# Performance work log

Measured on AMD Instinct MI355X. Metric: run time of the kernel, lower is better.

## Reference

```python
import jax, jax.numpy as jnp
import numpy as np

STEPS = 3


def setup_inputs() -> dict:
    key = jax.random.key(0)
    ks = jax.random.split(key, 6)
    N, H, B = 1000000, 128, 16384
    x = jax.random.normal(ks[0], (N, H), dtype=jnp.float32)
    batch_vec = jnp.sort(jax.random.randint(ks[1], (N,), 0, B)).astype(jnp.int64)
    scale_ih = 1.0 / np.sqrt(2 * H)
    scale_hh = 1.0 / np.sqrt(H)
    W_ih = jax.random.normal(ks[2], (4 * H, 2 * H), dtype=jnp.float32) * scale_ih
    W_hh = jax.random.normal(ks[3], (4 * H, H), dtype=jnp.float32) * scale_hh
    b_ih = jnp.zeros((4 * H,), dtype=jnp.float32)
    b_hh = jnp.zeros((4 * H,), dtype=jnp.float32)
    return {"x": x, "batch_vec": batch_vec, "W_ih": W_ih, "W_hh": W_hh,
            "b_ih": b_ih, "b_hh": b_hh, "num_graphs": B}


def _set2set(x, batch_vec, W_ih, W_hh, b_ih, b_hh, B):
    N, H = x.shape
    q_star = jnp.zeros((B, 2 * H), x.dtype)
    h = jnp.zeros((B, H), x.dtype)
    c = jnp.zeros((B, H), x.dtype)
    bias = b_ih + b_hh
    for _ in range(STEPS):
        # LSTMCell (torch gate order: i, f, g, o)
        gates = q_star @ W_ih.T + h @ W_hh.T + bias  # [B, 4H]
        i, f, g, o = jnp.split(gates, 4, axis=-1)
        c = jax.nn.sigmoid(f) * c + jax.nn.sigmoid(i) * jnp.tanh(g)
        h = jax.nn.sigmoid(o) * jnp.tanh(c)
        q = h  # [B, H]
        # attention logits per node
        e = jnp.sum(x * q[batch_vec], axis=-1)  # [N]
        emax = jax.ops.segment_max(e, batch_vec, num_segments=B)
        emax = jax.lax.stop_gradient(jnp.where(jnp.isfinite(emax), emax, 0.0))
        ex = jnp.exp(e - emax[batch_vec])
        denom = jax.ops.segment_sum(ex, batch_vec, num_segments=B)
        a = ex / denom[batch_vec]  # segment softmax, [N]
        r = jax.ops.segment_sum(a[:, None] * x, batch_vec, num_segments=B)  # [B, H]
        q_star = jnp.concatenate([q, r], axis=-1)  # [B, 2H]
    return q_star


def reference(x, batch_vec, W_ih, W_hh, b_ih, b_hh, num_graphs):
    return _set2set(x, batch_vec, W_ih, W_hh, b_ih, b_hh, int(num_graphs))
```

## Files before the change

### kernel.cpp

```cpp
#include <hip/hip_runtime.h>
#include <math.h>

#define HDIM 128
#define G4 512
#define TS 36

typedef float vf4 __attribute__((ext_vector_type(4)));
typedef unsigned short u16x8 __attribute__((ext_vector_type(8)));

__device__ __forceinline__ float sigm(float v) { return 1.0f / (1.0f + __expf(-v)); }
__device__ __forceinline__ float ftanh(float v) {
    return 1.0f - 2.0f / (__expf(2.0f * v) + 1.0f);
}
__device__ __forceinline__ float dot4(vf4 a, vf4 b) {
    return a.x * b.x + a.y * b.y + a.z * b.z + a.w * b.w;
}
__device__ __forceinline__ vf4 ldnt4(const float* p) {
    return __builtin_nontemporal_load((const vf4*)p);
}
__device__ __forceinline__ unsigned short f2bf(float f) {
    unsigned u = __float_as_uint(f);
    u += 0x7fff + ((u >> 16) & 1);
    return (unsigned short)(u >> 16);
}
__device__ __forceinline__ float bf2f(unsigned short h) {
    return __uint_as_float(((unsigned)h) << 16);
}

__global__ __launch_bounds__(256) void k_setup(const float* __restrict__ W_ih,
                                               const float* __restrict__ W_hh,
                                               const float* __restrict__ b_ih,
                                               const float* __restrict__ b_hh,
                                               const int* __restrict__ batch_vec, int N, int B,
                                               float* __restrict__ Wc, int* __restrict__ seg_start,
                                               float* __restrict__ gh0) {
    __shared__ float h0s[HDIM];
    int t = blockIdx.x * 256 + threadIdx.x;
    if (blockIdx.x < 2) {
        if (threadIdx.x < HDIM) {
            int hid = threadIdx.x;
            float bi = b_ih[hid] + b_hh[hid];
            float bg = b_ih[2 * HDIM + hid] + b_hh[2 * HDIM + hid];
            float bo = b_ih[3 * HDIM + hid] + b_hh[3 * HDIM + hid];
            float c0 = sigm(bi) * ftanh(bg);
            h0s[hid] = sigm(bo) * ftanh(c0);
        }
        __syncthreads();
        if (t < G4) {
            float s = 0.0f;
#pragma unroll
            for (int k = 0; k < HDIM; k += 4) {
                vf4 wi = *(const vf4*)(W_ih + (size_t)t * 256 + k);
                vf4 wh = *(const vf4*)(W_hh + (size_t)t * HDIM + k);
                s += (wi.x + wh.x) * h0s[k] + (wi.y + wh.y) * h0s[k + 1] +
                     (wi.z + wh.z) * h0s[k + 2] + (wi.w + wh.w) * h0s[k + 3];
            }
            gh0[t] = s;
        }
    }
    if (t < G4 * 2 * HDIM) {
        int g = t >> 8;
        int k = t & 255;
        float w = W_ih[g * 256 + k];
        if (k < HDIM) w += W_hh[g * HDIM + k];
        Wc[t] = w;
    }
    if (t <= B) {
        int lo = 0, hi = N;
        while (lo < hi) {
            int mid = (lo + hi) >> 1;
            if (batch_vec[mid] < t) lo = mid + 1; else hi = mid;
        }
        seg_start[t] = lo;
    }
}

#define UPD(m_, d_, ra_, rb_, p_, xa_, xb_)  \
    {                                        \
        float mn_ = fmaxf(m_, p_);           \
        float sc_ = __expf(m_ - mn_);        \
        float pe_ = __expf(p_ - mn_);        \
        d_ = d_ * sc_ + pe_;                 \
        ra_ = ra_ * sc_ + pe_ * xa_;         \
        rb_ = rb_ * sc_ + pe_ * xb_;         \
        m_ = mn_;                            \
    }

#define SHFL16(p_)                  \
    p_ += __shfl_xor(p_, 1, 64);    \
    p_ += __shfl_xor(p_, 2, 64);    \
    p_ += __shfl_xor(p_, 4, 64);    \
    p_ += __shfl_xor(p_, 8, 64);

struct AttState {
    float m0, d0, m1, d1;
    vf4 ra0, rb0, ra1, rb1;
};

__device__ __forceinline__ void init_state(AttState& st) {
    st.m0 = 0.f; st.d0 = 0.f; st.m1 = 0.f; st.d1 = 0.f;
    st.ra0 = vf4{0.f, 0.f, 0.f, 0.f}; st.rb0 = vf4{0.f, 0.f, 0.f, 0.f};
    st.ra1 = vf4{0.f, 0.f, 0.f, 0.f}; st.rb1 = vf4{0.f, 0.f, 0.f, 0.f};
}

__device__ __forceinline__ void compute4(const vf4 xa[4], const vf4 xb[4], int baserow, int e,
                                         vf4 qa, vf4 qb, AttState& st) {
    float p[4];
#pragma unroll
    for (int t = 0; t < 4; ++t) p[t] = dot4(xa[t], qa) + dot4(xb[t], qb);
    SHFL16(p[0]) SHFL16(p[1]) SHFL16(p[2]) SHFL16(p[3])
#pragma unroll
    for (int t = 0; t < 4; ++t)
        if (baserow + t >= e) p[t] = -1e30f;
    UPD(st.m0, st.d0, st.ra0, st.rb0, p[0], xa[0], xb[0])
    UPD(st.m1, st.d1, st.ra1, st.rb1, p[1], xa[1], xb[1])
    UPD(st.m0, st.d0, st.ra0, st.rb0, p[2], xa[2], xb[2])
    UPD(st.m1, st.d1, st.ra1, st.rb1, p[3], xa[3], xb[3])
}

__device__ __forceinline__ void finish_state(AttState& st, float* dst) {
    float M = fmaxf(st.m0, st.m1);
    float w0 = __expf(st.m0 - M), w1 = __expf(st.m1 - M);
    float d = st.d0 * w0 + st.d1 * w1;
    vf4 ra = st.ra0 * w0 + st.ra1 * w1;
    vf4 rb = st.rb0 * w0 + st.rb1 * w1;
    float inv = (d > 0.0f) ? 1.0f / d : 0.0f;
    *(vf4*)dst = ra * inv;
    *(vf4*)(dst + 4) = rb * inv;
}

__device__ __forceinline__ int seg_of_block(int bid, int nblk, int rev, int wave, int quarter) {
    int q8 = nblk >> 3, r8 = nblk & 7;
    int xcd = bid & 7, pos = bid >> 3;
    int nb = (xcd < r8 ? xcd * (q8 + 1) : r8 * (q8 + 1) + (xcd - r8) * q8) + pos;
    if (rev) nb = nblk - 1 - nb;
    return nb * 16 + wave * 4 + quarter;
}

__global__ __launch_bounds__(256) void k_attn_cvt(const float* __restrict__ x,
                                                  unsigned short* __restrict__ x16,
                                                  const float* __restrict__ b_ih,
                                                  const float* __restrict__ b_hh,
                                                  const int* __restrict__ seg_start,
                                                  float* __restrict__ r_out, int B) {
    int wave = threadIdx.x >> 6;
    int lane = threadIdx.x & 63;
    int l16 = lane & 15;
    int quarter = lane >> 4;
    int seg = seg_of_block(blockIdx.x, gridDim.x, 0, wave, quarter);
    int seg_c = min(seg, B - 1);
    int s = seg_start[seg_c], e = seg_start[seg_c + 1];
    if (seg >= B) { s = 0; e = 0; }

    vf4 qa, qb;
    {
        int c = l16 * 8;
        vf4 bi0 = *(const vf4*)(b_ih + c) + *(const vf4*)(b_hh + c);
        vf4 bi1 = *(const vf4*)(b_ih + c + 4) + *(const vf4*)(b_hh + c + 4);
        vf4 bg0 = *(const vf4*)(b_ih + 2 * HDIM + c) + *(const vf4*)(b_hh + 2 * HDIM + c);
        vf4 bg1 = *(const vf4*)(b_ih + 2 * HDIM + c + 4) + *(const vf4*)(b_hh + 2 * HDIM + c + 4);
        vf4 bo0 = *(const vf4*)(b_ih + 3 * HDIM + c) + *(const vf4*)(b_hh + 3 * HDIM + c);
        vf4 bo1 = *(const vf4*)(b_ih + 3 * HDIM + c + 4) + *(const vf4*)(b_hh + 3 * HDIM + c + 4);
#pragma unroll
        for (int j = 0; j < 4; ++j) {
            float c0 = sigm(bi0[j]) * ftanh(bg0[j]);
            qa[j] = sigm(bo0[j]) * ftanh(c0);
            float c1 = sigm(bi1[j]) * ftanh(bg1[j]);
            qb[j] = sigm(bo1[j]) * ftanh(c1);
        }
    }

    int iters = (e - s + 3) >> 2;
    iters = max(iters, __shfl_xor(iters, 16, 64));
    iters = max(iters, __shfl_xor(iters, 32, 64));
    iters = max(iters, 1);

    AttState st;
    init_state(st);

    vf4 ca[4], cb[4];
#pragma unroll
    for (int t = 0; t < 4; ++t) {
        int rl = max(min(s + t, e - 1), 0);
        const float* xr = x + (size_t)rl * HDIM + l16 * 8;
        ca[t] = ldnt4(xr);
        cb[t] = ldnt4(xr + 4);
    }
    int base = s;
#pragma unroll 1
    for (int j = 1; j < iters; ++j) {
        vf4 na[4], nb[4];
#pragma unroll
        for (int t = 0; t < 4; ++t) {
            int rl = max(min(s + 4 * j + t, e - 1), 0);
            const float* xr = x + (size_t)rl * HDIM + l16 * 8;
            na[t] = ldnt4(xr);
            nb[t] = ldnt4(xr + 4);
        }
#pragma unroll
        for (int t = 0; t < 4; ++t) {
            if (base + t < e) {
                u16x8 cv;
                cv[0] = f2bf(ca[t].x); cv[1] = f2bf(ca[t].y); cv[2] = f2bf(ca[t].z); cv[3] = f2bf(ca[t].w);
                cv[4] = f2bf(cb[t].x); cv[5] = f2bf(cb[t].y); cv[6] = f2bf(cb[t].z); cv[7] = f2bf(cb[t].w);
                *(u16x8*)(x16 + (size_t)(base + t) * HDIM + l16 * 8) = cv;
            }
        }
        compute4(ca, cb, base, e, qa, qb, st);
#pragma unroll
        for (int t = 0; t < 4; ++t) { ca[t] = na[t]; cb[t] = nb[t]; }
        base += 4;
    }
#pragma unroll
    for (int t = 0; t < 4; ++t) {
        if (base + t < e) {
            u16x8 cv;
            cv[0] = f2bf(ca[t].x); cv[1] = f2bf(ca[t].y); cv[2] = f2bf(ca[t].z); cv[3] = f2bf(ca[t].w);
            cv[4] = f2bf(cb[t].x); cv[5] = f2bf(cb[t].y); cv[6] = f2bf(cb[t].z); cv[7] = f2bf(cb[t].w);
            *(u16x8*)(x16 + (size_t)(base + t) * HDIM + l16 * 8) = cv;
        }
    }
    compute4(ca, cb, base, e, qa, qb, st);

    if (seg < B) finish_state(st, r_out + (size_t)seg * HDIM + l16 * 8);
}

__global__ __launch_bounds__(256) void k_attn_b16(const unsigned short* __restrict__ x16,
                                                  const float* __restrict__ q, int ldq,
                                                  const int* __restrict__ seg_start,
                                                  float* __restrict__ r_out, int ldr, int col_off,
                                                  int B, int rev) {
    int wave = threadIdx.x >> 6;
    int lane = threadIdx.x & 63;
    int l16 = lane & 15;
    int quarter = lane >> 4;
    int seg = seg_of_block(blockIdx.x, gridDim.x, rev, wave, quarter);
    int seg_c = min(seg, B - 1);
    int s = seg_start[seg_c], e = seg_start[seg_c + 1];
    if (seg >= B) { s = 0; e = 0; }

    const float* qrow = q + (size_t)seg_c * ldq + l16 * 8;
    vf4 qa = *(const vf4*)qrow;
    vf4 qb = *(const vf4*)(qrow + 4);

    int iters = (e - s + 3) >> 2;
    iters = max(iters, __shfl_xor(iters, 16, 64));
    iters = max(iters, __shfl_xor(iters, 32, 64));
    iters = max(iters, 1);

    AttState st;
    init_state(st);

    u16x8 cur[4];
#pragma unroll
    for (int t = 0; t < 4; ++t) {
        int rl = max(min(s + t, e - 1), 0);
        cur[t] = *(const u16x8*)(x16 + (size_t)rl * HDIM + l16 * 8);
    }
    int base = s;
#pragma unroll 1
    for (int j = 1; j < iters; ++j) {
        u16x8 nxt[4];
#pragma unroll
        for (int t = 0; t < 4; ++t) {
            int rl = max(min(s + 4 * j + t, e - 1), 0);
            nxt[t] = *(const u16x8*)(x16 + (size_t)rl * HDIM + l16 * 8);
        }
        vf4 xa[4], xb[4];
#pragma unroll
        for (int t = 0; t < 4; ++t) {
            xa[t] = vf4{bf2f(cur[t][0]), bf2f(cur[t][1]), bf2f(cur[t][2]), bf2f(cur[t][3])};
            xb[t] = vf4{bf2f(cur[t][4]), bf2f(cur[t][5]), bf2f(cur[t][6]), bf2f(cur[t][7])};
        }
        compute4(xa, xb, base, e, qa, qb, st);
#pragma unroll
        for (int t = 0; t < 4; ++t) cur[t] = nxt[t];
        base += 4;
    }
    {
        vf4 xa[4], xb[4];
#pragma unroll
        for (int t = 0; t < 4; ++t) {
            xa[t] = vf4{bf2f(cur[t][0]), bf2f(cur[t][1]), bf2f(cur[t][2]), bf2f(cur[t][3])};
            xb[t] = vf4{bf2f(cur[t][4]), bf2f(cur[t][5]), bf2f(cur[t][6]), bf2f(cur[t][7])};
        }
        compute4(xa, xb, base, e, qa, qb, st);
    }

    if (seg < B) finish_state(st, r_out + (size_t)seg * ldr + col_off + l16 * 8);
}

__global__ __launch_bounds__(256) void k_gemm_lstm1(const float* __restrict__ r_prev,
                                                    const float* __restrict__ Wc,
                                                    const float* __restrict__ gh0,
                                                    const float* __restrict__ b_ih,
                                                    const float* __restrict__ b_hh,
                                                    float* __restrict__ h_new,
                                                    float* __restrict__ c_new) {
    __shared__ float As[128 * TS];
    __shared__ float Ws[64 * TS];
    int ct = blockIdx.y;
    int rb = blockIdx.x * 128;
    int tid = threadIdx.x;
    int tx = tid & 15, ty = tid >> 4;
    float acc[8][4];
#pragma unroll
    for (int i = 0; i < 8; ++i)
#pragma unroll
        for (int j = 0; j < 4; ++j) acc[i][j] = 0.0f;

    for (int kc = 0; kc < 4; ++kc) {
        int kbase = kc * 32;
#pragma unroll
        for (int i = 0; i < 4; ++i) {
            int li = tid + i * 256;
            int row = li >> 3;
            int c4 = (li & 7) * 4;
            *(vf4*)&As[row * TS + c4] = *(const vf4*)(r_prev + (size_t)(rb + row) * HDIM + kbase + c4);
        }
#pragma unroll
        for (int i = 0; i < 2; ++i) {
            int li = tid + i * 256;
            int col = li >> 3;
            int c4 = (li & 7) * 4;
            int g = ct * 16 + (col & 15) + 128 * (col >> 4);
            *(vf4*)&Ws[col * TS + c4] = *(const vf4*)(Wc + (size_t)g * 256 + 128 + kbase + c4);
        }
        __syncthreads();
#pragma unroll
        for (int k = 0; k < 32; k += 4) {
            vf4 a[8], b[4];
#pragma unroll
            for (int i = 0; i < 8; ++i) a[i] = *(vf4*)&As[(ty + 16 * i) * TS + k];
#pragma unroll
            for (int j = 0; j < 4; ++j) b[j] = *(vf4*)&Ws[(tx + 16 * j) * TS + k];
#pragma unroll
            for (int i = 0; i < 8; ++i)
#pragma unroll
                for (int j = 0; j < 4; ++j) {
                    acc[i][j] += a[i].x * b[j].x + a[i].y * b[j].y +
                                 a[i].z * b[j].z + a[i].w * b[j].w;
                }
        }
        __syncthreads();
    }
    int hidx = ct * 16 + tx;
    float bi = b_ih[hidx] + b_hh[hidx] + gh0[hidx];
    float bf = b_ih[HDIM + hidx] + b_hh[HDIM + hidx] + gh0[HDIM + hidx];
    float bg = b_ih[2 * HDIM + hidx] + b_hh[2 * HDIM + hidx] + gh0[2 * HDIM + hidx];
    float bo = b_ih[3 * HDIM + hidx] + b_hh[3 * HDIM + hidx] + gh0[3 * HDIM + hidx];
    float bi0 = b_ih[hidx] + b_hh[hidx];
    float bg0 = b_ih[2 * HDIM + hidx] + b_hh[2 * HDIM + hidx];
    float c0 = sigm(bi0) * ftanh(bg0);
#pragma unroll
    for (int i = 0; i < 8; ++i) {
        int row = rb + ty + 16 * i;
        float gi = acc[i][0] + bi;
        float gf = acc[i][1] + bf;
        float gg = acc[i][2] + bg;
        float go = acc[i][3] + bo;
        float cn = sigm(gf) * c0 + sigm(gi) * ftanh(gg);
        float hn = sigm(go) * ftanh(cn);
        c_new[(size_t)row * HDIM + hidx] = cn;
        h_new[(size_t)row * HDIM + hidx] = hn;
    }
}

__global__ __launch_bounds__(256) void k_gemm_lstm(const float* __restrict__ h_prev,
                                                   const float* __restrict__ r_prev,
                                                   const float* __restrict__ c_prev,
                                                   const float* __restrict__ Wc,
                                                   const float* __restrict__ b_ih,
                                                   const float* __restrict__ b_hh,
                                                   float* __restrict__ h_mirror) {
    __shared__ float As[128 * TS];
    __shared__ float Ws[64 * TS];
    int ct = blockIdx.y;
    int rb = blockIdx.x * 128;
    int tid = threadIdx.x;
    int tx = tid & 15, ty = tid >> 4;
    float acc[8][4];
#pragma unroll
    for (int i = 0; i < 8; ++i)
#pragma unroll
        for (int j = 0; j < 4; ++j) acc[i][j] = 0.0f;

    for (int kc = 0; kc < 8; ++kc) {
        const float* src = (kc < 4) ? h_prev : r_prev;
        int kbase = (kc & 3) * 32;
#pragma unroll
        for (int i = 0; i < 4; ++i) {
            int li = tid + i * 256;
            int row = li >> 3;
            int c4 = (li & 7) * 4;
            *(vf4*)&As[row * TS + c4] = *(const vf4*)(src + (size_t)(rb + row) * HDIM + kbase + c4);
        }
#pragma unroll
        for (int i = 0; i < 2; ++i) {
            int li = tid + i * 256;
            int col = li >> 3;
            int c4 = (li & 7) * 4;
            int g = ct * 16 + (col & 15) + 128 * (col >> 4);
            *(vf4*)&Ws[col * TS + c4] = *(const vf4*)(Wc + (size_t)g * 256 + kc * 32 + c4);
        }
        __syncthreads();
#pragma unroll
        for (int k = 0; k < 32; k += 4) {
            vf4 a[8], b[4];
#pragma unroll
            for (int i = 0; i < 8; ++i) a[i] = *(vf4*)&As[(ty + 16 * i) * TS + k];
#pragma unroll
            for (int j = 0; j < 4; ++j) b[j] = *(vf4*)&Ws[(tx + 16 * j) * TS + k];
#pragma unroll
            for (int i = 0; i < 8; ++i)
#pragma unroll
                for (int j = 0; j < 4; ++j) {
                    acc[i][j] += a[i].x * b[j].x + a[i].y * b[j].y +
                                 a[i].z * b[j].z + a[i].w * b[j].w;
                }
        }
        __syncthreads();
    }
    int hidx = ct * 16 + tx;
    float bi = b_ih[hidx] + b_hh[hidx];
    float bf = b_ih[HDIM + hidx] + b_hh[HDIM + hidx];
    float bg = b_ih[2 * HDIM + hidx] + b_hh[2 * HDIM + hidx];
    float bo = b_ih[3 * HDIM + hidx] + b_hh[3 * HDIM + hidx];
#pragma unroll
    for (int i = 0; i < 8; ++i) {
        int row = rb + ty + 16 * i;
        float gi = acc[i][0] + bi;
        float gf = acc[i][1] + bf;
        float gg = acc[i][2] + bg;
        float go = acc[i][3] + bo;
        float cp = c_prev[(size_t)row * HDIM + hidx];
        float cn = sigm(gf) * cp + sigm(gi) * ftanh(gg);
        float hn = sigm(go) * ftanh(cn);
        h_mirror[(size_t)row * 2 * HDIM + hidx] = hn;
    }
}

extern "C" void kernel_launch(void* const* d_in, const int* in_sizes, int n_in,
                              void* d_out, int out_size, void* d_ws, size_t ws_size,
                              hipStream_t stream) {
    const float* x = (const float*)d_in[0];
    const int* batch_vec = (const int*)d_in[1];
    const float* W_ih = (const float*)d_in[2];
    const float* W_hh = (const float*)d_in[3];
    const float* b_ih = (const float*)d_in[4];
    const float* b_hh = (const float*)d_in[5];
    float* out = (float*)d_out;

    int N = in_sizes[1];
    int B = out_size / (2 * HDIM);

    char* ws = (char*)d_ws;
    float* Wc = (float*)ws;            ws += (size_t)G4 * 2 * HDIM * 4;
    float* gh0 = (float*)ws;           ws += (size_t)G4 * 4;
    float* h_b = (float*)ws;           ws += (size_t)B * HDIM * 4;
    float* cbuf = (float*)ws;          ws += (size_t)B * HDIM * 4;
    float* rbuf = (float*)ws;          ws += (size_t)B * HDIM * 4;
    int* seg = (int*)ws;               ws += (size_t)(B + 1) * 4;
    ws = (char*)(((size_t)ws + 255) & ~(size_t)255);
    unsigned short* x16 = (unsigned short*)ws;

    k_setup<<<512, 256, 0, stream>>>(W_ih, W_hh, b_ih, b_hh, batch_vec, N, B, Wc, seg, gh0);

    dim3 ggrid(B / 128, 8);
    int ablk = (B + 15) / 16;
    k_attn_cvt<<<ablk, 256, 0, stream>>>(x, x16, b_ih, b_hh, seg, rbuf, B);
    k_gemm_lstm1<<<ggrid, 256, 0, stream>>>(rbuf, Wc, gh0, b_ih, b_hh, h_b, cbuf);
    k_attn_b16<<<ablk, 256, 0, stream>>>(x16, h_b, HDIM, seg, rbuf, HDIM, 0, B, 1);
    k_gemm_lstm<<<ggrid, 256, 0, stream>>>(h_b, rbuf, cbuf, Wc, b_ih, b_hh, out);
    k_attn_b16<<<ablk, 256, 0, stream>>>(x16, out, 2 * HDIM, seg, out, 2 * HDIM, HDIM, B, 0);
}
```

Before: 456.4 us.

## Partition attention by fixed node slabs with atomic merging of straddling segments

Replaces the one-segment-per-16-lane-group attention kernels with kernels where each wave processes a fixed slab of 256 consecutive nodes and walks the segment boundaries inside it. Segments entirely inside a slab are written directly, and segments that cross slabs are merged with atomic adds into raw numerator and denominator buffers. Normalization moves into the following GEMM loads and a final small normalize kernel. This targets load imbalance from variable segment sizes and the padding waste in quarter-wave groups. In exchange it drops max-subtraction in the softmax, so exp can overflow on large logits, and it adds a memset, atomics and an extra kernel.

```diff
diff --git a/kernel.cpp b/kernel.cpp
--- a/kernel.cpp
+++ b/kernel.cpp
@@ -4,6 +4,8 @@
 #define HDIM 128
 #define G4 512
 #define TS 36
+#define SLAB 256
+#define WIN 16
 
 typedef float vf4 __attribute__((ext_vector_type(4)));
 typedef unsigned short u16x8 __attribute__((ext_vector_type(8)));
@@ -26,6 +28,12 @@
 __device__ __forceinline__ float bf2f(unsigned short h) {
     return __uint_as_float(((unsigned)h) << 16);
 }
+
+#define SHFL16(p_)                  \
+    p_ += __shfl_xor(p_, 1, 64);    \
+    p_ += __shfl_xor(p_, 2, 64);    \
+    p_ += __shfl_xor(p_, 4, 64);    \
+    p_ += __shfl_xor(p_, 8, 64);
 
 __global__ __launch_bounds__(256) void k_setup(const float* __restrict__ W_ih,
                                                const float* __restrict__ W_hh,
@@ -75,82 +83,59 @@
     }
 }
 
-#define UPD(m_, d_, ra_, rb_, p_, xa_, xb_)  \
-    {                                        \
-        float mn_ = fmaxf(m_, p_);           \
-        float sc_ = __expf(m_ - mn_);        \
-        float pe_ = __expf(p_ - mn_);        \
-        d_ = d_ * sc_ + pe_;                 \
-        ra_ = ra_ * sc_ + pe_ * xa_;         \
-        rb_ = rb_ * sc_ + pe_ * xb_;         \
-        m_ = mn_;                            \
-    }
-
-#define SHFL16(p_)                  \
-    p_ += __shfl_xor(p_, 1, 64);    \
-    p_ += __shfl_xor(p_, 2, 64);    \
-    p_ += __shfl_xor(p_, 4, 64);    \
-    p_ += __shfl_xor(p_, 8, 64);
-
-struct AttState {
-    float m0, d0, m1, d1;
-    vf4 ra0, rb0, ra1, rb1;
-};
-
-__device__ __forceinline__ void init_state(AttState& st) {
-    st.m0 = 0.f; st.d0 = 0.f; st.m1 = 0.f; st.d1 = 0.f;
-    st.ra0 = vf4{0.f, 0.f, 0.f, 0.f}; st.rb0 = vf4{0.f, 0.f, 0.f, 0.f};
-    st.ra1 = vf4{0.f, 0.f, 0.f, 0.f}; st.rb1 = vf4{0.f, 0.f, 0.f, 0.f};
-}
-
-__device__ __forceinline__ void compute4(const vf4 xa[4], const vf4 xb[4], int baserow, int e,
-                                         vf4 qa, vf4 qb, AttState& st) {
-    float p[4];
-#pragma unroll
-    for (int t = 0; t < 4; ++t) p[t] = dot4(xa[t], qa) + dot4(xb[t], qb);
-    SHFL16(p[0]) SHFL16(p[1]) SHFL16(p[2]) SHFL16(p[3])
-#pragma unroll
-    for (int t = 0; t < 4; ++t)
-        if (baserow + t >= e) p[t] = -1e30f;
-    UPD(st.m0, st.d0, st.ra0, st.rb0, p[0], xa[0], xb[0])
-    UPD(st.m1, st.d1, st.ra1, st.rb1, p[1], xa[1], xb[1])
-    UPD(st.m0, st.d0, st.ra0, st.rb0, p[2], xa[2], xb[2])
-    UPD(st.m1, st.d1, st.ra1, st.rb1, p[3], xa[3], xb[3])
-}
-
-__device__ __forceinline__ void finish_state(AttState& st, float* dst) {
-    float M = fmaxf(st.m0, st.m1);
-    float w0 = __expf(st.m0 - M), w1 = __expf(st.m1 - M);
-    float d = st.d0 * w0 + st.d1 * w1;
-    vf4 ra = st.ra0 * w0 + st.ra1 * w1;
-    vf4 rb = st.rb0 * w0 + st.rb1 * w1;
-    float inv = (d > 0.0f) ? 1.0f / d : 0.0f;
-    *(vf4*)dst = ra * inv;
-    *(vf4*)(dst + 4) = rb * inv;
-}
-
-__device__ __forceinline__ int seg_of_block(int bid, int nblk, int rev, int wave, int quarter) {
-    int q8 = nblk >> 3, r8 = nblk & 7;
-    int xcd = bid & 7, pos = bid >> 3;
-    int nb = (xcd < r8 ? xcd * (q8 + 1) : r8 * (q8 + 1) + (xcd - r8) * q8) + pos;
-    if (rev) nb = nblk - 1 - nb;
-    return nb * 16 + wave * 4 + quarter;
-}
-
-__global__ __launch_bounds__(256) void k_attn_cvt(const float* __restrict__ x,
-                                                  unsigned short* __restrict__ x16,
-                                                  const float* __restrict__ b_ih,
-                                                  const float* __restrict__ b_hh,
-                                                  const int* __restrict__ seg_start,
-                                                  float* __restrict__ r_out, int B) {
-    int wave = threadIdx.x >> 6;
-    int lane = threadIdx.x & 63;
-    int l16 = lane & 15;
-    int quarter = lane >> 4;
-    int seg = seg_of_block(blockIdx.x, gridDim.x, 0, wave, quarter);
-    int seg_c = min(seg, B - 1);
-    int s = seg_start[seg_c], e = seg_start[seg_c + 1];
-    if (seg >= B) { s = 0; e = 0; }
+__device__ __forceinline__ void flush_seg(int seg, int segLo, int segend, int r0, int r1,
+                                          float d, vf4 ra, vf4 rb,
+                                          float* __restrict__ r_raw, float* __restrict__ d_raw,
+                                          int l16, int quarter) {
+#pragma unroll
+    for (int off = 16; off <= 32; off <<= 1) {
+        d += __shfl_xor(d, off, 64);
+        ra.x += __shfl_xor(ra.x, off, 64);
+        ra.y += __shfl_xor(ra.y, off, 64);
+        ra.z += __shfl_xor(ra.z, off, 64);
+        ra.w += __shfl_xor(ra.w, off, 64);
+        rb.x += __shfl_xor(rb.x, off, 64);
+        rb.y += __shfl_xor(rb.y, off, 64);
+        rb.z += __shfl_xor(rb.z, off, 64);
+        rb.w += __shfl_xor(rb.w, off, 64);
+    }
+    if (quarter != 0) return;
+    float* rp = r_raw + (size_t)seg * HDIM + l16 * 8;
+    if (segLo >= r0 && segend <= r1) {
+        float inv = d > 0.f ? 1.f / d : 0.f;
+        *(vf4*)rp = ra * inv;
+        *(vf4*)(rp + 4) = rb * inv;
+        if (l16 == 0) d_raw[seg] = 1.0f;
+    } else {
+#pragma unroll
+        for (int j = 0; j < 4; ++j) {
+            atomicAdd(rp + j, ra[j]);
+            atomicAdd(rp + 4 + j, rb[j]);
+        }
+        if (l16 == 0) atomicAdd(d_raw + seg, d);
+    }
+}
+
+__global__ __launch_bounds__(256) void k_attn_lin32(const float* __restrict__ x,
+                                                    unsigned short* __restrict__ x16,
+                                                    const float* __restrict__ b_ih,
+                                                    const float* __restrict__ b_hh,
+                                                    const int* __restrict__ seg_start,
+                                                    float* __restrict__ r_raw,
+                                                    float* __restrict__ d_raw, int N, int B) {
+    int wave = threadIdx.x >> 6, lane = threadIdx.x & 63;
+    int l16 = lane & 15, quarter = lane >> 4;
+    int wid = blockIdx.x * 4 + wave;
+    int r0 = wid * SLAB;
+    if (r0 >= N) return;
+    int r1 = min(r0 + SLAB, N);
+
+    int lo = 0, hi = B - 1;
+    while (lo < hi) { int mid = (lo + hi + 1) >> 1; if (seg_start[mid] <= r0) lo = mid; else hi = mid - 1; }
+    int seg = lo;
+    int segLo = seg_start[seg];
+    int segend = seg_start[seg + 1];
+    int lowB = r0;
 
     vf4 qa, qb;
     {
@@ -170,101 +155,110 @@
         }
     }
 
-    int iters = (e - s + 3) >> 2;
-    iters = max(iters, __shfl_xor(iters, 16, 64));
-    iters = max(iters, __shfl_xor(iters, 32, 64));
-    iters = max(iters, 1);
-
-    AttState st;
-    init_state(st);
-
+    float d = 0.f; vf4 ra = {0, 0, 0, 0}, rb = {0, 0, 0, 0};
+    int nwin = (r1 - r0 + WIN - 1) / WIN;
     vf4 ca[4], cb[4];
 #pragma unroll
     for (int t = 0; t < 4; ++t) {
-        int rl = max(min(s + t, e - 1), 0);
-        const float* xr = x + (size_t)rl * HDIM + l16 * 8;
+        int row = min(r0 + quarter + 4 * t, r1 - 1);
+        const float* xr = x + (size_t)row * HDIM + l16 * 8;
         ca[t] = ldnt4(xr);
         cb[t] = ldnt4(xr + 4);
     }
-    int base = s;
 #pragma unroll 1
-    for (int j = 1; j < iters; ++j) {
+    for (int wnd = 0; wnd < nwin; ++wnd) {
+        int base = r0 + wnd * WIN;
+        int we = min(base + WIN, r1);
         vf4 na[4], nb[4];
+        if (wnd + 1 < nwin) {
+#pragma unroll
+            for (int t = 0; t < 4; ++t) {
+                int row = min(base + WIN + quarter + 4 * t, r1 - 1);
+                const float* xr = x + (size_t)row * HDIM + l16 * 8;
+                na[t] = ldnt4(xr);
+                nb[t] = ldnt4(xr + 4);
+            }
+        }
 #pragma unroll
         for (int t = 0; t < 4; ++t) {
-            int rl = max(min(s + 4 * j + t, e - 1), 0);
-            const float* xr = x + (size_t)rl * HDIM + l16 * 8;
-            na[t] = ldnt4(xr);
-            nb[t] = ldnt4(xr + 4);
-        }
-#pragma unroll
-        for (int t = 0; t < 4; ++t) {
-            if (base + t < e) {
+            int row = base + quarter + 4 * t;
+            if (row < we) {
                 u16x8 cv;
                 cv[0] = f2bf(ca[t].x); cv[1] = f2bf(ca[t].y); cv[2] = f2bf(ca[t].z); cv[3] = f2bf(ca[t].w);
                 cv[4] = f2bf(cb[t].x); cv[5] = f2bf(cb[t].y); cv[6] = f2bf(cb[t].z); cv[7] = f2bf(cb[t].w);
-                *(u16x8*)(x16 + (size_t)(base + t) * HDIM + l16 * 8) = cv;
-            }
-        }
-        compute4(ca, cb, base, e, qa, qb, st);
+                *(u16x8*)(x16 + (size_t)row * HDIM + l16 * 8) = cv;
+            }
+        }
+#pragma unroll 1
+        while (true) {
+            float p[4];
+#pragma unroll
+            for (int t = 0; t < 4; ++t) p[t] = dot4(ca[t], qa) + dot4(cb[t], qb);
+            SHFL16(p[0]) SHFL16(p[1]) SHFL16(p[2]) SHFL16(p[3])
+#pragma unroll
+            for (int t = 0; t < 4; ++t) {
+                int row = base + quarter + 4 * t;
+                float w = (row >= lowB && row < segend && row < we) ? __expf(p[t]) : 0.f;
+                d += w;
+                ra += w * ca[t];
+                rb += w * cb[t];
+            }
+            if (segend >= we) break;
+            flush_seg(seg, segLo, segend, r0, r1, d, ra, rb, r_raw, d_raw, l16, quarter);
+            lowB = segend; segLo = segend;
+            ++seg;
+            segend = seg_start[seg + 1];
+            d = 0.f; ra = vf4{0, 0, 0, 0}; rb = vf4{0, 0, 0, 0};
+        }
 #pragma unroll
         for (int t = 0; t < 4; ++t) { ca[t] = na[t]; cb[t] = nb[t]; }
-        base += 4;
-    }
+    }
+    flush_seg(seg, segLo, segend, r0, r1, d, ra, rb, r_raw, d_raw, l16, quarter);
+}
+
+__global__ __launch_bounds__(256) void k_attn_lin16(const unsigned short* __restrict__ x16,
+                                                    const float* __restrict__ q, int ldq,
+                                                    const int* __restrict__ seg_start,
+                                                    float* __restrict__ r_raw,
+                                                    float* __restrict__ d_raw, int N, int B) {
+    int wave = threadIdx.x >> 6, lane = threadIdx.x & 63;
+    int l16 = lane & 15, quarter = lane >> 4;
+    int wid = blockIdx.x * 4 + wave;
+    int r0 = wid * SLAB;
+    if (r0 >= N) return;
+    int r1 = min(r0 + SLAB, N);
+
+    int lo = 0, hi = B - 1;
+    while (lo < hi) { int mid = (lo + hi + 1) >> 1; if (seg_start[mid] <= r0) lo = mid; else hi = mid - 1; }
+    int seg = lo;
+    int segLo = seg_start[seg];
+    int segend = seg_start[seg + 1];
+    int lowB = r0;
+
+    vf4 qa, qb;
+    {
+        const float* qr = q + (size_t)seg * ldq + l16 * 8;
+        qa = *(const vf4*)qr; qb = *(const vf4*)(qr + 4);
+    }
+
+    float d = 0.f; vf4 ra = {0, 0, 0, 0}, rb = {0, 0, 0, 0};
+    int nwin = (r1 - r0 + WIN - 1) / WIN;
+    u16x8 cur[4], nxt[4];
 #pragma unroll
     for (int t = 0; t < 4; ++t) {
-        if (base + t < e) {
-            u16x8 cv;
-            cv[0] = f2bf(ca[t].x); cv[1] = f2bf(ca[t].y); cv[2] = f2bf(ca[t].z); cv[3] = f2bf(ca[t].w);
-            cv[4] = f2bf(cb[t].x); cv[5] = f2bf(cb[t].y); cv[6] = f2bf(cb[t].z); cv[7] = f2bf(cb[t].w);
-            *(u16x8*)(x16 + (size_t)(base + t) * HDIM + l16 * 8) = cv;
-        }
-    }
-    compute4(ca, cb, base, e, qa, qb, st);
-
-    if (seg < B) finish_state(st, r_out + (size_t)seg * HDIM + l16 * 8);
-}
-
-__global__ __launch_bounds__(256) void k_attn_b16(const unsigned short* __restrict__ x16,
-                                                  const float* __restrict__ q, int ldq,
-                                                  const int* __restrict__ seg_start,
-                                                  float* __restrict__ r_out, int ldr, int col_off,
-                                                  int B, int rev) {
-    int wave = threadIdx.x >> 6;
-    int lane = threadIdx.x & 63;
-    int l16 = lane & 15;
-    int quarter = lane >> 4;
-    int seg = seg_of_block(blockIdx.x, gridDim.x, rev, wave, quarter);
-    int seg_c = min(seg, B - 1);
-    int s = seg_start[seg_c], e = seg_start[seg_c + 1];
-    if (seg >= B) { s = 0; e = 0; }
-
-    const float* qrow = q + (size_t)seg_c * ldq + l16 * 8;
-    vf4 qa = *(const vf4*)qrow;
-    vf4 qb = *(const vf4*)(qrow + 4);
-
-    int iters = (e - s + 3) >> 2;
-    iters = max(iters, __shfl_xor(iters, 16, 64));
-    iters = max(iters, __shfl_xor(iters, 32, 64));
-    iters = max(iters, 1);
-
-    AttState st;
-    init_state(st);
-
-    u16x8 cur[4];
-#pragma unroll
-    for (int t = 0; t < 4; ++t) {
-        int rl = max(min(s + t, e - 1), 0);
-        cur[t] = *(const u16x8*)(x16 + (size_t)rl * HDIM + l16 * 8);
-    }
-    int base = s;
+        int row = min(r0 + quarter + 4 * t, r1 - 1);
+        cur[t] = *(const u16x8*)(x16 + (size_t)row * HDIM + l16 * 8);
+    }
 #pragma unroll 1
-    for (int j = 1; j < iters; ++j) {
-        u16x8 nxt[4];
-#pragma unroll
-        for (int t = 0; t < 4; ++t) {
-            int rl = max(min(s + 4 * j + t, e - 1), 0);
-            nxt[t] = *(const u16x8*)(x16 + (size_t)rl * HDIM + l16 * 8);
+    for (int wnd = 0; wnd < nwin; ++wnd) {
+        int base = r0 + wnd * WIN;
+        int we = min(base + WIN, r1);
+        if (wnd + 1 < nwin) {
+#pragma unroll
+            for (int t = 0; t < 4; ++t) {
+                int row = min(base + WIN + quarter + 4 * t, r1 - 1);
+                nxt[t] = *(const u16x8*)(x16 + (size_t)row * HDIM + l16 * 8);
+            }
         }
         vf4 xa[4], xb[4];
 #pragma unroll
@@ -272,25 +266,39 @@
             xa[t] = vf4{bf2f(cur[t][0]), bf2f(cur[t][1]), bf2f(cur[t][2]), bf2f(cur[t][3])};
             xb[t] = vf4{bf2f(cur[t][4]), bf2f(cur[t][5]), bf2f(cur[t][6]), bf2f(cur[t][7])};
         }
-        compute4(xa, xb, base, e, qa, qb, st);
+#pragma unroll 1
+        while (true) {
+            float p[4];
+#pragma unroll
+            for (int t = 0; t < 4; ++t) p[t] = dot4(xa[t], qa) + dot4(xb[t], qb);
+            SHFL16(p[0]) SHFL16(p[1]) SHFL16(p[2]) SHFL16(p[3])
+#pragma unroll
+            for (int t = 0; t < 4; ++t) {
+                int row = base + quarter + 4 * t;
+                float w = (row >= lowB && row < segend && row < we) ? __expf(p[t]) : 0.f;
+                d += w;
+                ra += w * xa[t];
+                rb += w * xb[t];
+            }
+            if (segend >= we) break;
+            flush_seg(seg, segLo, segend, r0, r1, d, ra, rb, r_raw, d_raw, l16, quarter);
+            lowB = segend; segLo = segend;
+            ++seg;
+            segend = seg_start[seg + 1];
+            {
+                const float* qr = q + (size_t)seg * ldq + l16 * 8;
+                qa = *(const vf4*)qr; qb = *(const vf4*)(qr + 4);
+            }
+            d = 0.f; ra = vf4{0, 0, 0, 0}; rb = vf4{0, 0, 0, 0};
+        }
 #pragma unroll
         for (int t = 0; t < 4; ++t) cur[t] = nxt[t];
-        base += 4;
-    }
-    {
-        vf4 xa[4], xb[4];
-#pragma unroll
-        for (int t = 0; t < 4; ++t) {
-            xa[t] = vf4{bf2f(cur[t][0]), bf2f(cur[t][1]), bf2f(cur[t][2]), bf2f(cur[t][3])};
-            xb[t] = vf4{bf2f(cur[t][4]), bf2f(cur[t][5]), bf2f(cur[t][6]), bf2f(cur[t][7])};
-        }
-        compute4(xa, xb, base, e, qa, qb, st);
-    }
-
-    if (seg < B) finish_state(st, r_out + (size_t)seg * ldr + col_off + l16 * 8);
-}
-
-__global__ __launch_bounds__(256) void k_gemm_lstm1(const float* __restrict__ r_prev,
+    }
+    flush_seg(seg, segLo, segend, r0, r1, d, ra, rb, r_raw, d_raw, l16, quarter);
+}
+
+__global__ __launch_bounds__(256) void k_gemm_lstm1(const float* __restrict__ r_raw,
+                                                    const float* __restrict__ d_raw,
                                                     const float* __restrict__ Wc,
                                                     const float* __restrict__ gh0,
                                                     const float* __restrict__ b_ih,
@@ -299,10 +307,16 @@
                                                     float* __restrict__ c_new) {
     __shared__ float As[128 * TS];
     __shared__ float Ws[64 * TS];
+    __shared__ float ds[128];
     int ct = blockIdx.y;
     int rb = blockIdx.x * 128;
     int tid = threadIdx.x;
     int tx = tid & 15, ty = tid >> 4;
+    if (tid < 128) {
+        float dv = d_raw[rb + tid];
+        ds[tid] = dv > 0.f ? 1.f / dv : 0.f;
+    }
+    __syncthreads();
     float acc[8][4];
 #pragma unroll
     for (int i = 0; i < 8; ++i)
@@ -316,7 +330,8 @@
             int li = tid + i * 256;
             int row = li >> 3;
             int c4 = (li & 7) * 4;
-            *(vf4*)&As[row * TS + c4] = *(const vf4*)(r_prev + (size_t)(rb + row) * HDIM + kbase + c4);
+            vf4 v = *(const vf4*)(r_raw + (size_t)(rb + row) * HDIM + kbase + c4);
+            *(vf4*)&As[row * TS + c4] = v * ds[row];
         }
 #pragma unroll
         for (int i = 0; i < 2; ++i) {
@@ -367,7 +382,8 @@
 }
 
 __global__ __launch_bounds__(256) void k_gemm_lstm(const float* __restrict__ h_prev,
-                                                   const float* __restrict__ r_prev,
+                                                   const float* __restrict__ r_raw,
+                                                   const float* __restrict__ d_raw,
                                                    const float* __restrict__ c_prev,
                                                    const float* __restrict__ Wc,
                                                    const float* __restrict__ b_ih,
@@ -375,10 +391,16 @@
                                                    float* __restrict__ h_mirror) {
     __shared__ float As[128 * TS];
     __shared__ float Ws[64 * TS];
+    __shared__ float ds[128];
     int ct = blockIdx.y;
     int rb = blockIdx.x * 128;
     int tid = threadIdx.x;
     int tx = tid & 15, ty = tid >> 4;
+    if (tid < 128) {
+        float dv = d_raw[rb + tid];
+        ds[tid] = dv > 0.f ? 1.f / dv : 0.f;
+    }
+    __syncthreads();
     float acc[8][4];
 #pragma unroll
     for (int i = 0; i < 8; ++i)
@@ -386,14 +408,16 @@
         for (int j = 0; j < 4; ++j) acc[i][j] = 0.0f;
 
     for (int kc = 0; kc < 8; ++kc) {
-        const float* src = (kc < 4) ? h_prev : r_prev;
+        const float* src = (kc < 4) ? h_prev : r_raw;
         int kbase = (kc & 3) * 32;
 #pragma unroll
         for (int i = 0; i < 4; ++i) {
             int li = tid + i * 256;
             int row = li >> 3;
             int c4 = (li & 7) * 4;
-            *(vf4*)&As[row * TS + c4] = *(const vf4*)(src + (size_t)(rb + row) * HDIM + kbase + c4);
+            vf4 v = *(const vf4*)(src + (size_t)(rb + row) * HDIM + kbase + c4);
+            if (kc >= 4) v *= ds[row];
+            *(vf4*)&As[row * TS + c4] = v;
         }
 #pragma unroll
         for (int i = 0; i < 2; ++i) {
@@ -440,6 +464,17 @@
     }
 }
 
+__global__ __launch_bounds__(256) void k_norm(const float* __restrict__ r_raw,
+                                              const float* __restrict__ d_raw,
+                                              float* __restrict__ out, int B) {
+    int idx = blockIdx.x * 256 + threadIdx.x;
+    if (idx >= B * HDIM) return;
+    int seg = idx >> 7, c = idx & 127;
+    float dv = d_raw[seg];
+    float inv = dv > 0.f ? 1.f / dv : 0.f;
+    out[(size_t)seg * 2 * HDIM + HDIM + c] = r_raw[idx] * inv;
+}
+
 extern "C" void kernel_launch(void* const* d_in, const int* in_sizes, int n_in,
                               void* d_out, int out_size, void* d_ws, size_t ws_size,
                               hipStream_t stream) {
@@ -455,22 +490,34 @@
     int B = out_size / (2 * HDIM);
 
     char* ws = (char*)d_ws;
-    float* Wc = (float*)ws;            ws += (size_t)G4 * 2 * HDIM * 4;
-    float* gh0 = (float*)ws;           ws += (size_t)G4 * 4;
-    float* h_b = (float*)ws;           ws += (size_t)B * HDIM * 4;
-    float* cbuf = (float*)ws;          ws += (size_t)B * HDIM * 4;
-    float* rbuf = (float*)ws;          ws += (size_t)B * HDIM * 4;
-    int* seg = (int*)ws;               ws += (size_t)(B + 1) * 4;
+    float* Wc = (float*)ws;   ws += (size_t)G4 * 2 * HDIM * 4;
+    float* gh0 = (float*)ws;  ws += (size_t)G4 * 4;
+    float* h_b = (float*)ws;  ws += (size_t)B * HDIM * 4;
+    float* cbuf = (float*)ws; ws += (size_t)B * HDIM * 4;
+    int* seg = (int*)ws;      ws += (size_t)(B + 1) * 4;
+    ws = (char*)(((size_t)ws + 255) & ~(size_t)255);
+    char* raw_base = ws;
+    float* rA = (float*)ws;   ws += (size_t)B * HDIM * 4;
+    float* rB = (float*)ws;   ws += (size_t)B * HDIM * 4;
+    float* rC = (float*)ws;   ws += (size_t)B * HDIM * 4;
+    float* dA = (float*)ws;   ws += (size_t)B * 4;
+    float* dB = (float*)ws;   ws += (size_t)B * 4;
+    float* dC = (float*)ws;   ws += (size_t)B * 4;
+    size_t raw_bytes = (size_t)(ws - raw_base);
     ws = (char*)(((size_t)ws + 255) & ~(size_t)255);
     unsigned short* x16 = (unsigned short*)ws;
 
+    hipMemsetAsync(raw_base, 0, raw_bytes, stream);
     k_setup<<<512, 256, 0, stream>>>(W_ih, W_hh, b_ih, b_hh, batch_vec, N, B, Wc, seg, gh0);
 
+    int nwaves = (N + SLAB - 1) / SLAB;
+    int ablk = (nwaves + 3) / 4;
     dim3 ggrid(B / 128, 8);
-    int ablk = (B + 15) / 16;
-    k_attn_cvt<<<ablk, 256, 0, stream>>>(x, x16, b_ih, b_hh, seg, rbuf, B);
-    k_gemm_lstm1<<<ggrid, 256, 0, stream>>>(rbuf, Wc, gh0, b_ih, b_hh, h_b, cbuf);
-    k_attn_b16<<<ablk, 256, 0, stream>>>(x16, h_b, HDIM, seg, rbuf, HDIM, 0, B, 1);
-    k_gemm_lstm<<<ggrid, 256, 0, stream>>>(h_b, rbuf, cbuf, Wc, b_ih, b_hh, out);
-    k_attn_b16<<<ablk, 256, 0, stream>>>(x16, out, 2 * HDIM, seg, out, 2 * HDIM, HDIM, B, 0);
-}
+
+    k_attn_lin32<<<ablk, 256, 0, stream>>>(x, x16, b_ih, b_hh, seg, rA, dA, N, B);
+    k_gemm_lstm1<<<ggrid, 256, 0, stream>>>(rA, dA, Wc, gh0, b_ih, b_hh, h_b, cbuf);
+    k_attn_lin16<<<ablk, 256, 0, stream>>>(x16, h_b, HDIM, seg, rB, dB, N, B);
+    k_gemm_lstm<<<ggrid, 256, 0, stream>>>(h_b, rB, dB, cbuf, Wc, b_ih, b_hh, out);
+    k_attn_lin16<<<ablk, 256, 0, stream>>>(x16, out, 2 * HDIM, seg, rC, dC, N, B);
+    k_norm<<<(B * HDIM + 255) / 256, 256, 0, stream>>>(rC, dC, out, B);
+}
```

Result: slower. 594.1 us (+30.2%).
